# Optimization experiments

Measured on AMD Instinct MI355X. Metric: run time of the kernel, lower is better.

The kernel has to match this reference:

```python
import jax, jax.numpy as jnp
import numpy as np

CURV = 1.0          # manifold curvature c
HEADS = 4
HEAD_DIM = 32       # (dim-1) // heads = 128 // 4
SCALE = HEAD_DIM ** -0.5
EPS = 1e-7

N_NODES = 50000
N_EDGES = 800000
D = 128             # tangent feature dim (dim - 1)


def log_origin(x, c):
    """Lorentz log map at the origin o=(1/sqrt(c),0,...); returns spatial (d) part of tangent."""
    sc = jnp.sqrt(c)
    x0 = x[..., 0]
    xs = x[..., 1:]
    norm = jnp.sqrt(jnp.sum(xs * xs, axis=-1) + EPS)         # (N,)
    dist = jnp.arccosh(jnp.maximum(sc * x0, 1.0 + EPS)) / sc  # (N,)
    return (dist / norm)[..., None] * xs                      # (N, d)


def exp_origin(vs, c):
    """Lorentz exp map at origin of tangent vector (0, vs); returns point (N, d+1)."""
    sc = jnp.sqrt(c)
    r = jnp.sqrt(jnp.sum(vs * vs, axis=-1) + EPS)  # (N,)
    arg = sc * r
    x0 = jnp.cosh(arg) / sc
    xs = (jnp.sinh(arg) / arg)[..., None] * vs
    return jnp.concatenate([x0[..., None], xs], axis=-1)


def setup_inputs() -> dict:
    key = jax.random.key(0)
    k1, k2, k3, k4, k5, k6, k7 = jax.random.split(key, 7)
    # valid hyperboloid points: x0 = sqrt(1/c + ||xs||^2)
    xs = 0.5 * jax.random.normal(k1, (N_NODES, D), dtype=jnp.float32)
    x0 = jnp.sqrt(1.0 / CURV + jnp.sum(xs * xs, axis=-1, keepdims=True))
    x = jnp.concatenate([x0, xs], axis=-1)  # (N, d+1)
    edge_index = jax.random.randint(k2, (2, N_EDGES), 0, N_NODES, dtype=jnp.int64)
    s = D ** -0.5
    Wq = s * jax.random.normal(k3, (D, D), dtype=jnp.float32)
    Wk = s * jax.random.normal(k4, (D, D), dtype=jnp.float32)
    Wv = s * jax.random.normal(k5, (D, D), dtype=jnp.float32)
    Wo = s * jax.random.normal(k6, (D, D), dtype=jnp.float32)
    bo = jnp.zeros((D,), dtype=jnp.float32)
    return {"x": x, "edge_index": edge_index, "Wq": Wq, "Wk": Wk, "Wv": Wv, "Wo": Wo, "bo": bo}


def reference(x, edge_index, Wq, Wk, Wv, Wo, bo):
    N = x.shape[0]
    row, col = edge_index[0], edge_index[1]
    # map to tangent space at origin, drop the (zero) time component
    x_tan = log_origin(x, CURV)                       # (N, d)
    Q = (x_tan @ Wq.T).reshape(N, HEADS, HEAD_DIM)
    K = (x_tan @ Wk.T).reshape(N, HEADS, HEAD_DIM)
    V = (x_tan @ Wv.T).reshape(N, HEADS, HEAD_DIM)
    # per-edge attention logits, grouped softmax over incoming edges of each target node (col)
    scores = jnp.einsum('ehd,ehd->eh', Q[col], K[row]) * SCALE   # (E, H)
    m = jax.ops.segment_max(scores, col, num_segments=N)         # (N, H)
    e = jnp.exp(scores - m[col])
    denom = jax.ops.segment_sum(e, col, num_segments=N)          # (N, H)
    att = e / denom[col]                                         # (E, H)
    # weighted scatter-sum of values
    agg = jax.ops.segment_sum(att[..., None] * V[row], col, num_segments=N)  # (N, H, hd)
    agg = agg.reshape(N, HEADS * HEAD_DIM)
    out = agg @ Wo.T + bo                                        # (N, d)
    # lift back: prepend zero time component, exp map at origin
    return exp_origin(out, CURV)                                 # (N, d+1)
```

## Files before the change

kernel.cpp:

```cpp
#include <hip/hip_runtime.h>
#include <hip/hip_fp8.h>
#include <math.h>

#define EPS 1e-7f
#define SCALE 0.17677669529663687f
#define MAXDEG 64
#define BIN_EPT 16
#define BIN_EDGES 4096
#define BUCK_CAP 5120
#define NBUCK_MAX 256

typedef _Float16 half2v __attribute__((ext_vector_type(2)));
typedef _Float16 f16x4 __attribute__((ext_vector_type(4)));
typedef _Float16 f16x8 __attribute__((ext_vector_type(8)));
typedef float f32x4 __attribute__((ext_vector_type(4)));
typedef float f32x2 __attribute__((ext_vector_type(2)));

__device__ __forceinline__ void gload16(const void* g, void* l) {
  __builtin_amdgcn_global_load_lds(
      (const __attribute__((address_space(1))) unsigned int*)g,
      (__attribute__((address_space(3))) unsigned int*)l, 16, 0, 0);
}

__global__ __launch_bounds__(256) void zero_cnt(int* __restrict__ bcnt, int n) {
  int i = blockIdx.x * 256 + threadIdx.x;
  if (i < n) bcnt[i] = 0;
}

__global__ __launch_bounds__(256) void prep_kernel(
    const float* __restrict__ x,
    const float* __restrict__ Wq, const float* __restrict__ Wk,
    const float* __restrict__ Wv, const float* __restrict__ Wo,
    _Float16* __restrict__ Wc, _Float16* __restrict__ Wof,
    _Float16* __restrict__ xt,
    const int* __restrict__ col, const int* __restrict__ row,
    unsigned* __restrict__ staging, int* __restrict__ bcnt,
    int bin_nb, int nbuck, int E, int N) {
  __shared__ int hist[NBUCK_MAX];
  __shared__ int rbase[NBUCK_MAX];
  int b = blockIdx.x;
  int tid = threadIdx.x;
  if (b < bin_nb) {
    int e0 = b * BIN_EDGES;
    if (tid < nbuck) hist[tid] = 0;
    __syncthreads();
    int bkt[BIN_EPT], rk[BIN_EPT];
    unsigned pk[BIN_EPT];
#pragma unroll
    for (int j = 0; j < BIN_EPT; j++) {
      int e = e0 + j * 256 + tid;
      if (e < E) {
        int c = col[e];
        int r = row[e];
        int bb = c >> 8;
        bkt[j] = bb;
        pk[j] = ((unsigned)(c & 255) << 16) | (unsigned)r;
        rk[j] = atomicAdd(&hist[bb], 1);
      } else {
        bkt[j] = -1;
        rk[j] = 0;
        pk[j] = 0;
      }
    }
    __syncthreads();
    if (tid < nbuck) rbase[tid] = atomicAdd(&bcnt[tid], hist[tid]);
    __syncthreads();
#pragma unroll
    for (int j = 0; j < BIN_EPT; j++) {
      if (bkt[j] >= 0) {
        int slot = rbase[bkt[j]] + rk[j];
        if (slot < BUCK_CAP)
          staging[(size_t)bkt[j] * BUCK_CAP + slot] = pk[j];
      }
    }
    return;
  }
  b -= bin_nb;
  if (b < 256) {
    int o = b * 256 + tid;
    int j = o >> 7;
    int i = o & 127;
    if (j < 384) {
      const float* W = (j < 128) ? Wq : (j < 256) ? Wk : Wv;
      Wc[o] = (_Float16)W[(j & 127) * 128 + i];
    } else {
      Wof[(j - 384) * 128 + i] = (_Float16)Wo[(j - 384) * 128 + i];
    }
    return;
  }
  int node = (b - 256) * 4 + (tid >> 6);
  if (node >= N) return;
  int lane = tid & 63;
  float2 xs = *reinterpret_cast<const float2*>(&x[(size_t)node * 129 + 1 + lane * 2]);
  float ss = fmaf(xs.x, xs.x, xs.y * xs.y);
#pragma unroll
  for (int o = 32; o >= 1; o >>= 1) ss += __shfl_xor(ss, o, 64);
  float norm = sqrtf(ss + EPS);
  float x0 = x[(size_t)node * 129];
  float xm = fmaxf(x0, 1.0f + EPS);
  float dist = __logf(xm + sqrtf(fmaxf(fmaf(xm, xm, -1.0f), 0.0f)));
  float sc = dist / norm;
  half2v h;
  h.x = (_Float16)(sc * xs.x);
  h.y = (_Float16)(sc * xs.y);
  *reinterpret_cast<half2v*>(&xt[(size_t)node * 128 + lane * 2]) = h;
}

template <int NCHUNKS, int MODE>
__global__ __launch_bounds__(256, 3) void gemm_mfma(
    const _Float16* __restrict__ A,
    const _Float16* __restrict__ B,
    void* __restrict__ C0, void* __restrict__ C1,
    const float* __restrict__ bias, int M,
    const unsigned* __restrict__ staging, const int* __restrict__ bcnt,
    unsigned short* __restrict__ rml, int* __restrict__ cnt, int Mblocks) {
  __shared__ _Float16 Bs[128 * 128];
  __shared__ __align__(16) unsigned char Cs[16384];
  const int bid = blockIdx.x;
  const int tid = threadIdx.x;

  if (MODE == 0 && bid >= Mblocks) {
    int bk = bid - Mblocks;
    unsigned short* slab = (unsigned short*)Bs;
    int* lc = (int*)Cs;
    lc[tid] = 0;
    __syncthreads();
    int ec = bcnt[bk];
    if (ec > BUCK_CAP) ec = BUCK_CAP;
    const unsigned* sg = staging + (size_t)bk * BUCK_CAP;
    for (int i = tid; i < ec; i += 256) {
      unsigned p = sg[i];
      int nl = p >> 16;
      int pos = atomicAdd(&lc[nl], 1);
      if (pos < MAXDEG) slab[nl * MAXDEG + pos] = (unsigned short)(p & 0xFFFF);
    }
    __syncthreads();
    uint4* gs = (uint4*)(rml + (size_t)bk * 256 * MAXDEG);
    const uint4* ls = (const uint4*)slab;
#pragma unroll
    for (int i = 0; i < 8; i++) gs[i * 256 + tid] = ls[i * 256 + tid];
    int c = lc[tid];
    cnt[bk * 256 + tid] = (c > MAXDEG) ? MAXDEG : c;
    return;
  }

  const int wave = tid >> 6;
  const int lane = tid & 63;
  const int wm = wave >> 1, wn = wave & 1;
  const int lrow = lane & 15, q = lane >> 4;
  const int m0 = bid * 64;

#pragma unroll
  for (int j = 0; j < 4; j++) {
    int slot0 = (j * 4 + wave) * 64;
    int p = slot0 + lane;
    int m = p >> 4;
    int kcl = (p & 15) ^ (m & 15);
    int msrc = m0 + m;
    if (msrc > M - 1) msrc = M - 1;
    gload16(A + (size_t)msrc * 128 + kcl * 8, (char*)Bs + (size_t)slot0 * 16);
  }
  __syncthreads();

  f16x8 afr[2][4];
  {
    const f16x8* Av = (const f16x8*)Bs;
#pragma unroll
    for (int mt = 0; mt < 2; mt++) {
      int m = wm * 32 + mt * 16 + lrow;
#pragma unroll
      for (int s = 0; s < 4; s++) {
        int kc = s * 4 + q;
        afr[mt][s] = Av[m * 16 + (kc ^ (m & 15))];
      }
    }
  }
  __syncthreads();

  auto stageB = [&](int c) {
#pragma unroll
    for (int j = 0; j < 8; j++) {
      int slot0 = (j * 4 + wave) * 64;
      int p = slot0 + lane;
      int n = p >> 4;
      int kcl = (p & 15) ^ (n & 15);
      gload16(B + ((size_t)(c * 128 + n)) * 128 + kcl * 8, (char*)Bs + (size_t)slot0 * 16);
    }
  };
  stageB(0);

  f32x4 acc[2][4];
  for (int c = 0; c < NCHUNKS; c++) {
    __syncthreads();

#pragma unroll
    for (int mt = 0; mt < 2; mt++)
#pragma unroll
      for (int nt = 0; nt < 4; nt++) acc[mt][nt] = (f32x4)0.f;

    const f16x8* Bv = (const f16x8*)Bs;
#pragma unroll
    for (int s = 0; s < 4; s++) {
      int kc = s * 4 + q;
      f16x8 bf[4];
#pragma unroll
      for (int nt = 0; nt < 4; nt++) {
        int n = wn * 64 + nt * 16 + lrow;
        bf[nt] = Bv[n * 16 + (kc ^ (n & 15))];
      }
#pragma unroll
      for (int mt = 0; mt < 2; mt++)
#pragma unroll
        for (int nt = 0; nt < 4; nt++)
          acc[mt][nt] = __builtin_amdgcn_mfma_f32_16x16x32_f16(afr[mt][s], bf[nt], acc[mt][nt], 0, 0, 0);
    }

    if (MODE == 0) {
      if (c == 0) {
#pragma unroll
        for (int mt = 0; mt < 2; mt++)
#pragma unroll
          for (int reg = 0; reg < 4; reg++) {
            int r = wm * 32 + mt * 16 + q * 4 + reg;
            int sw = ((r >> 2) & 3) << 5;
#pragma unroll
            for (int nt = 0; nt < 4; nt++) {
              int cl = wn * 64 + nt * 16 + lrow;
              *(_Float16*)(Cs + r * 256 + ((cl * 2) ^ sw)) = (_Float16)acc[mt][nt][reg];
            }
          }
      } else {
        unsigned char* cb = Cs + ((c == 2) ? 8192 : 0);
#pragma unroll
        for (int mt = 0; mt < 2; mt++) {
          int rb = wm * 32 + mt * 16 + q * 4;
          int sw = ((rb >> 2) & 3) << 5;
#pragma unroll
          for (int nt = 0; nt < 4; nt++) {
            int cl = wn * 64 + nt * 16 + lrow;
            int co = cl ^ sw;
            int p01 = __builtin_amdgcn_cvt_pk_fp8_f32(acc[mt][nt][0], acc[mt][nt][1], 0, false);
            int p23 = __builtin_amdgcn_cvt_pk_fp8_f32(acc[mt][nt][2], acc[mt][nt][3], 0, false);
            cb[(rb + 0) * 128 + co] = (unsigned char)(p01);
            cb[(rb + 1) * 128 + co] = (unsigned char)(p01 >> 8);
            cb[(rb + 2) * 128 + co] = (unsigned char)(p23);
            cb[(rb + 3) * 128 + co] = (unsigned char)(p23 >> 8);
          }
        }
      }
    }
    __syncthreads();
    if (c + 1 < NCHUNKS) stageB(c + 1);
    if (MODE == 0) {
      if (c == 0) {
#pragma unroll
        for (int it = 0; it < 4; it++) {
          int off = it * 4096 + tid * 16;
          int r = off >> 8;
          int bo = off & 255;
          int sw = ((r >> 2) & 3) << 5;
          uint4 v = *(const uint4*)(Cs + r * 256 + (bo ^ sw));
          int rg = m0 + r;
          if (rg < M) *(uint4*)((char*)C0 + (size_t)rg * 256 + bo) = v;
        }
      } else if (c == 2) {
#pragma unroll
        for (int it = 0; it < 8; it++) {
          int off = it * 2048 + tid * 8;
          int r = off >> 8;
          int u4 = (off & 255) >> 1;
          int sw = ((r >> 2) & 3) << 5;
          unsigned kw = *(const unsigned*)(Cs + r * 128 + (u4 ^ sw));
          unsigned vw = *(const unsigned*)(Cs + 8192 + r * 128 + (u4 ^ sw));
          int rg = m0 + r;
          if (rg < M) {
            uint2 o;
            o.x = kw;
            o.y = vw;
            *(uint2*)((char*)C1 + (size_t)rg * 256 + (off & 255)) = o;
          }
        }
      }
    }
  }

  if (MODE == 1) {
    float* out = (float*)C0;
    float* rsum = (float*)Cs;
#pragma unroll
    for (int mt = 0; mt < 2; mt++)
#pragma unroll
      for (int nt = 0; nt < 4; nt++) {
        int cl = wn * 64 + nt * 16 + lrow;
        float b = bias[cl];
#pragma unroll
        for (int reg = 0; reg < 4; reg++) acc[mt][nt][reg] += b;
      }
#pragma unroll
    for (int mt = 0; mt < 2; mt++) {
#pragma unroll
      for (int reg = 0; reg < 4; reg++) {
        float s4 = 0.f;
#pragma unroll
        for (int nt = 0; nt < 4; nt++) s4 = fmaf(acc[mt][nt][reg], acc[mt][nt][reg], s4);
#pragma unroll
        for (int o = 8; o >= 1; o >>= 1) s4 += __shfl_xor(s4, o, 16);
        if (lrow == 0) rsum[(wm * 32 + mt * 16 + q * 4 + reg) * 2 + wn] = s4;
      }
    }
    __syncthreads();
#pragma unroll
    for (int mt = 0; mt < 2; mt++) {
#pragma unroll
      for (int reg = 0; reg < 4; reg++) {
        int rl = wm * 32 + mt * 16 + q * 4 + reg;
        int rg = m0 + rl;
        if (rg < M) {
          float tot = rsum[rl * 2] + rsum[rl * 2 + 1];
          float r = sqrtf(tot + EPS);
          float er = __expf(r);
          float em = __expf(-r);
          float s = (er - em) * 0.5f / r;
#pragma unroll
          for (int nt = 0; nt < 4; nt++) {
            int cl = wn * 64 + nt * 16 + lrow;
            out[(size_t)rg * 129 + 1 + cl] = s * acc[mt][nt][reg];
          }
          if (wn == 0 && lrow == 0) out[(size_t)rg * 129] = (er + em) * 0.5f;
        }
      }
    }
  }
}

__global__ __launch_bounds__(256) void attn_kernel(
    const _Float16* __restrict__ Qb,
    const unsigned char* __restrict__ KVI,
    const unsigned short* __restrict__ rml, const int* __restrict__ cnt,
    _Float16* __restrict__ agg, int N) {
  int node = blockIdx.x * 4 + (threadIdx.x >> 6);
  if (node >= N) return;
  int lane = threadIdx.x & 63;
  int par = lane >> 5;
  int hd = lane & 31;
  int qoff = hd * 4;
  f16x4 qh = *reinterpret_cast<const f16x4*>(Qb + (size_t)node * 128 + qoff);
  float q0 = (float)qh[0], q1 = (float)qh[1], q2 = (float)qh[2], q3 = (float)qh[3];
  int deg = cnt[node];
  if (deg > MAXDEG) deg = MAXDEG;
  int eid = (int)rml[(size_t)node * MAXDEG + lane];
  float l = 0.f, av0 = 0.f, av1 = 0.f, av2 = 0.f, av3 = 0.f;

  auto dot = [&](uint2 w, float& p, float& v0, float& v1, float& v2, float& v3) {
    f32x2 k01 = __builtin_amdgcn_cvt_pk_f32_fp8((int)w.x, false);
    f32x2 k23 = __builtin_amdgcn_cvt_pk_f32_fp8((int)w.x, true);
    f32x2 va = __builtin_amdgcn_cvt_pk_f32_fp8((int)w.y, false);
    f32x2 vb = __builtin_amdgcn_cvt_pk_f32_fp8((int)w.y, true);
    v0 = va[0]; v1 = va[1]; v2 = vb[0]; v3 = vb[1];
    p = fmaf(q0, k01[0], fmaf(q1, k01[1], fmaf(q2, k23[0], q3 * k23[1])));
  };
  auto ld = [&](int r) {
    return *reinterpret_cast<const uint2*>(KVI + (size_t)r * 256 + hd * 8);
  };
  auto accum4 = [&](uint2 wA, uint2 wB, uint2 wC, uint2 wD) {
    float pA, a4, a5, a6, a7;
    float pB, b4, b5, b6, b7;
    float pC, c4, c5, c6, c7;
    float pD, d4, d5, d6, d7;
    dot(wA, pA, a4, a5, a6, a7);
    dot(wB, pB, b4, b5, b6, b7);
    dot(wC, pC, c4, c5, c6, c7);
    dot(wD, pD, d4, d5, d6, d7);
#pragma unroll
    for (int o = 4; o >= 1; o >>= 1) {
      pA += __shfl_xor(pA, o, 8);
      pB += __shfl_xor(pB, o, 8);
      pC += __shfl_xor(pC, o, 8);
      pD += __shfl_xor(pD, o, 8);
    }
    float eA = __expf(pA * SCALE);
    float eB = __expf(pB * SCALE);
    float eC = __expf(pC * SCALE);
    float eD = __expf(pD * SCALE);
    l += (eA + eB) + (eC + eD);
    av0 = fmaf(eA, a4, av0); av0 = fmaf(eB, b4, av0);
    av1 = fmaf(eA, a5, av1); av1 = fmaf(eB, b5, av1);
    av2 = fmaf(eA, a6, av2); av2 = fmaf(eB, b6, av2);
    av3 = fmaf(eA, a7, av3); av3 = fmaf(eB, b7, av3);
    av0 = fmaf(eC, c4, av0); av0 = fmaf(eD, d4, av0);
    av1 = fmaf(eC, c5, av1); av1 = fmaf(eD, d5, av1);
    av2 = fmaf(eC, c6, av2); av2 = fmaf(eD, d6, av2);
    av3 = fmaf(eC, c7, av3); av3 = fmaf(eD, d7, av3);
  };

  int i = 0;
  for (; i + 16 <= deg; i += 16) {
    int rA = __shfl(eid, i + par, 64);
    int rB = __shfl(eid, i + 2 + par, 64);
    int rC = __shfl(eid, i + 4 + par, 64);
    int rD = __shfl(eid, i + 6 + par, 64);
    int rE = __shfl(eid, i + 8 + par, 64);
    int rF = __shfl(eid, i + 10 + par, 64);
    int rG = __shfl(eid, i + 12 + par, 64);
    int rH = __shfl(eid, i + 14 + par, 64);
    uint2 wA = ld(rA);
    uint2 wB = ld(rB);
    uint2 wC = ld(rC);
    uint2 wD = ld(rD);
    uint2 wE = ld(rE);
    uint2 wF = ld(rF);
    uint2 wG = ld(rG);
    uint2 wH = ld(rH);
    accum4(wA, wB, wC, wD);
    accum4(wE, wF, wG, wH);
  }
  for (; i + 8 <= deg; i += 8) {
    int rA = __shfl(eid, i + par, 64);
    int rB = __shfl(eid, i + 2 + par, 64);
    int rC = __shfl(eid, i + 4 + par, 64);
    int rD = __shfl(eid, i + 6 + par, 64);
    uint2 wA = ld(rA);
    uint2 wB = ld(rB);
    uint2 wC = ld(rC);
    uint2 wD = ld(rD);
    accum4(wA, wB, wC, wD);
  }
  for (; i + 2 <= deg; i += 2) {
    int rA = __shfl(eid, i + par, 64);
    uint2 wA = ld(rA);
    float pA, a4, a5, a6, a7;
    dot(wA, pA, a4, a5, a6, a7);
#pragma unroll
    for (int o = 4; o >= 1; o >>= 1) pA += __shfl_xor(pA, o, 8);
    float eA = __expf(pA * SCALE);
    l += eA;
    av0 = fmaf(eA, a4, av0);
    av1 = fmaf(eA, a5, av1);
    av2 = fmaf(eA, a6, av2);
    av3 = fmaf(eA, a7, av3);
  }
  if (i < deg) {
    int r = __shfl(eid, i, 64);
    uint2 wA = ld(r);
    float pA, a4, a5, a6, a7;
    dot(wA, pA, a4, a5, a6, a7);
#pragma unroll
    for (int o = 4; o >= 1; o >>= 1) pA += __shfl_xor(pA, o, 8);
    float e = __expf(pA * SCALE) * (par ? 0.f : 1.f);
    l += e;
    av0 = fmaf(e, a4, av0);
    av1 = fmaf(e, a5, av1);
    av2 = fmaf(e, a6, av2);
    av3 = fmaf(e, a7, av3);
  }
  l += __shfl_xor(l, 32, 64);
  av0 += __shfl_xor(av0, 32, 64);
  av1 += __shfl_xor(av1, 32, 64);
  av2 += __shfl_xor(av2, 32, 64);
  av3 += __shfl_xor(av3, 32, 64);
  if (par == 0) {
    float inv = (l > 0.f) ? 1.0f / l : 0.f;
    f16x4 o4;
    o4[0] = (_Float16)(av0 * inv);
    o4[1] = (_Float16)(av1 * inv);
    o4[2] = (_Float16)(av2 * inv);
    o4[3] = (_Float16)(av3 * inv);
    *reinterpret_cast<f16x4*>(agg + (size_t)node * 128 + qoff) = o4;
  }
}

extern "C" void kernel_launch(void* const* d_in, const int* in_sizes, int n_in,
                              void* d_out, int out_size, void* d_ws, size_t ws_size,
                              hipStream_t stream) {
  const float* x = (const float*)d_in[0];
  const int* ei = (const int*)d_in[1];
  const float* Wq = (const float*)d_in[2];
  const float* Wk = (const float*)d_in[3];
  const float* Wv = (const float*)d_in[4];
  const float* Wo = (const float*)d_in[5];
  const float* bo = (const float*)d_in[6];
  float* out = (float*)d_out;

  const int N = in_sizes[0] / 129;
  const int E = in_sizes[1] / 2;
  const int* row = ei;
  const int* col = ei + E;

  const int nbuck = (N + 255) >> 8;
  const int bin_nb = (E + BIN_EDGES - 1) / BIN_EDGES;

  char* ws = (char*)d_ws;
  size_t off = 0;
  auto alloc = [&](size_t bytes) -> void* {
    off = (off + 255) & ~(size_t)255;
    void* p = ws + off;
    off += bytes;
    return p;
  };
  _Float16* xtan = (_Float16*)alloc((size_t)N * 128 * 2);
  _Float16* qbuf = (_Float16*)alloc((size_t)N * 128 * 2);
  unsigned char* kvi = (unsigned char*)alloc((size_t)N * 256);
  unsigned short* rml = (unsigned short*)alloc((size_t)nbuck * 256 * MAXDEG * 2);
  int* cnt        = (int*)alloc((size_t)nbuck * 256 * 4);
  unsigned* staging = (unsigned*)alloc((size_t)nbuck * BUCK_CAP * 4);
  int* bcnt       = (int*)alloc((size_t)nbuck * 4);
  _Float16* Wc    = (_Float16*)alloc(384 * 128 * 2);
  _Float16* Wof   = (_Float16*)alloc(128 * 128 * 2);

  const int gemm_nb = (N + 63) / 64;

  zero_cnt<<<(nbuck + 255) / 256, 256, 0, stream>>>(bcnt, nbuck);
  prep_kernel<<<bin_nb + 256 + (N + 3) / 4, 256, 0, stream>>>(
      x, Wq, Wk, Wv, Wo, Wc, Wof, xtan, col, row, staging, bcnt, bin_nb, nbuck,
      E, N);
  gemm_mfma<3, 0><<<gemm_nb + nbuck, 256, 0, stream>>>(
      xtan, Wc, qbuf, kvi, nullptr, N, staging, bcnt, rml, cnt, gemm_nb);
  attn_kernel<<<(N + 3) / 4, 256, 0, stream>>>(qbuf, kvi, rml, cnt, xtan, N);
  gemm_mfma<1, 1><<<gemm_nb, 256, 0, stream>>>(
      xtan, Wof, out, nullptr, bo, N, nullptr, nullptr, nullptr, nullptr, 0);
}
```

Before: 163.7 us.

## Replace global bucket atomics with per-block cells, drop zero kernel, unstage Wo in output GEMM

New measurement: 180.1 us. 10.0% more time.

```diff
diff --git a/kernel.cpp b/kernel.cpp
--- a/kernel.cpp
+++ b/kernel.cpp
@@ -7,7 +7,7 @@
 #define MAXDEG 64
 #define BIN_EPT 16
 #define BIN_EDGES 4096
-#define BUCK_CAP 5120
+#define CELL_CAP 64
 #define NBUCK_MAX 256
 
 typedef _Float16 half2v __attribute__((ext_vector_type(2)));
@@ -20,11 +20,6 @@
   __builtin_amdgcn_global_load_lds(
       (const __attribute__((address_space(1))) unsigned int*)g,
       (__attribute__((address_space(3))) unsigned int*)l, 16, 0, 0);
-}
-
-__global__ __launch_bounds__(256) void zero_cnt(int* __restrict__ bcnt, int n) {
-  int i = blockIdx.x * 256 + threadIdx.x;
-  if (i < n) bcnt[i] = 0;
 }
 
 __global__ __launch_bounds__(256) void prep_kernel(
@@ -34,10 +29,9 @@
     _Float16* __restrict__ Wc, _Float16* __restrict__ Wof,
     _Float16* __restrict__ xt,
     const int* __restrict__ col, const int* __restrict__ row,
-    unsigned* __restrict__ staging, int* __restrict__ bcnt,
+    unsigned* __restrict__ staging, int* __restrict__ ccnt,
     int bin_nb, int nbuck, int E, int N) {
   __shared__ int hist[NBUCK_MAX];
-  __shared__ int rbase[NBUCK_MAX];
   int b = blockIdx.x;
   int tid = threadIdx.x;
   if (b < bin_nb) {
@@ -63,14 +57,11 @@
       }
     }
     __syncthreads();
-    if (tid < nbuck) rbase[tid] = atomicAdd(&bcnt[tid], hist[tid]);
-    __syncthreads();
+    if (tid < nbuck) ccnt[b * NBUCK_MAX + tid] = hist[tid];
 #pragma unroll
     for (int j = 0; j < BIN_EPT; j++) {
-      if (bkt[j] >= 0) {
-        int slot = rbase[bkt[j]] + rk[j];
-        if (slot < BUCK_CAP)
-          staging[(size_t)bkt[j] * BUCK_CAP + slot] = pk[j];
+      if (bkt[j] >= 0 && rk[j] < CELL_CAP) {
+        staging[((size_t)bkt[j] * bin_nb + b) * CELL_CAP + rk[j]] = pk[j];
       }
     }
     return;
@@ -88,22 +79,27 @@
     }
     return;
   }
-  int node = (b - 256) * 4 + (tid >> 6);
+  int node = (b - 256) * 8 + (tid >> 5);
   if (node >= N) return;
-  int lane = tid & 63;
-  float2 xs = *reinterpret_cast<const float2*>(&x[(size_t)node * 129 + 1 + lane * 2]);
-  float ss = fmaf(xs.x, xs.x, xs.y * xs.y);
-#pragma unroll
-  for (int o = 32; o >= 1; o >>= 1) ss += __shfl_xor(ss, o, 64);
+  int sub = tid & 31;
+  const float* xr = x + (size_t)node * 129;
+  float2 xs01 = *reinterpret_cast<const float2*>(xr + 1 + sub * 4);
+  float2 xs23 = *reinterpret_cast<const float2*>(xr + 3 + sub * 4);
+  float ss = fmaf(xs01.x, xs01.x, xs01.y * xs01.y);
+  ss = fmaf(xs23.x, xs23.x, ss);
+  ss = fmaf(xs23.y, xs23.y, ss);
+#pragma unroll
+  for (int o = 16; o >= 1; o >>= 1) ss += __shfl_xor(ss, o, 64);
   float norm = sqrtf(ss + EPS);
-  float x0 = x[(size_t)node * 129];
-  float xm = fmaxf(x0, 1.0f + EPS);
+  float xm = fmaxf(xr[0], 1.0f + EPS);
   float dist = __logf(xm + sqrtf(fmaxf(fmaf(xm, xm, -1.0f), 0.0f)));
   float sc = dist / norm;
-  half2v h;
-  h.x = (_Float16)(sc * xs.x);
-  h.y = (_Float16)(sc * xs.y);
-  *reinterpret_cast<half2v*>(&xt[(size_t)node * 128 + lane * 2]) = h;
+  f16x4 h;
+  h[0] = (_Float16)(sc * xs01.x);
+  h[1] = (_Float16)(sc * xs01.y);
+  h[2] = (_Float16)(sc * xs23.x);
+  h[3] = (_Float16)(sc * xs23.y);
+  *reinterpret_cast<f16x4*>(&xt[(size_t)node * 128 + sub * 4]) = h;
 }
 
 template <int NCHUNKS, int MODE>
@@ -112,9 +108,10 @@
     const _Float16* __restrict__ B,
     void* __restrict__ C0, void* __restrict__ C1,
     const float* __restrict__ bias, int M,
-    const unsigned* __restrict__ staging, const int* __restrict__ bcnt,
-    unsigned short* __restrict__ rml, int* __restrict__ cnt, int Mblocks) {
-  __shared__ _Float16 Bs[128 * 128];
+    const unsigned* __restrict__ staging, const int* __restrict__ ccnt,
+    unsigned short* __restrict__ rml, int* __restrict__ cnt, int Mblocks,
+    int bin_nb) {
+  __shared__ _Float16 Bs[(MODE == 0) ? 128 * 128 : 64 * 128];
   __shared__ __align__(16) unsigned char Cs[16384];
   const int bid = blockIdx.x;
   const int tid = threadIdx.x;
@@ -125,14 +122,18 @@
     int* lc = (int*)Cs;
     lc[tid] = 0;
     __syncthreads();
-    int ec = bcnt[bk];
-    if (ec > BUCK_CAP) ec = BUCK_CAP;
-    const unsigned* sg = staging + (size_t)bk * BUCK_CAP;
-    for (int i = tid; i < ec; i += 256) {
-      unsigned p = sg[i];
-      int nl = p >> 16;
-      int pos = atomicAdd(&lc[nl], 1);
-      if (pos < MAXDEG) slab[nl * MAXDEG + pos] = (unsigned short)(p & 0xFFFF);
+    const unsigned* sg = staging + (size_t)bk * bin_nb * CELL_CAP;
+    int total = bin_nb * CELL_CAP;
+    for (int i = tid; i < total; i += 256) {
+      int blk = i >> 6;
+      int slot = i & (CELL_CAP - 1);
+      int ec = ccnt[blk * NBUCK_MAX + bk];
+      if (slot < ec) {
+        unsigned p = sg[i];
+        int nl = p >> 16;
+        int pos = atomicAdd(&lc[nl], 1);
+        if (pos < MAXDEG) slab[nl * MAXDEG + pos] = (unsigned short)(p & 0xFFFF);
+      }
     }
     __syncthreads();
     uint4* gs = (uint4*)(rml + (size_t)bk * 256 * MAXDEG);
@@ -175,30 +176,14 @@
       }
     }
   }
-  __syncthreads();
-
-  auto stageB = [&](int c) {
-#pragma unroll
-    for (int j = 0; j < 8; j++) {
-      int slot0 = (j * 4 + wave) * 64;
-      int p = slot0 + lane;
-      int n = p >> 4;
-      int kcl = (p & 15) ^ (n & 15);
-      gload16(B + ((size_t)(c * 128 + n)) * 128 + kcl * 8, (char*)Bs + (size_t)slot0 * 16);
-    }
-  };
-  stageB(0);
 
   f32x4 acc[2][4];
-  for (int c = 0; c < NCHUNKS; c++) {
-    __syncthreads();
-
+
+  if (MODE == 1) {
 #pragma unroll
     for (int mt = 0; mt < 2; mt++)
 #pragma unroll
       for (int nt = 0; nt < 4; nt++) acc[mt][nt] = (f32x4)0.f;
-
-    const f16x8* Bv = (const f16x8*)Bs;
 #pragma unroll
     for (int s = 0; s < 4; s++) {
       int kc = s * 4 + q;
@@ -206,7 +191,7 @@
 #pragma unroll
       for (int nt = 0; nt < 4; nt++) {
         int n = wn * 64 + nt * 16 + lrow;
-        bf[nt] = Bv[n * 16 + (kc ^ (n & 15))];
+        bf[nt] = *reinterpret_cast<const f16x8*>(B + (size_t)n * 128 + kc * 8);
       }
 #pragma unroll
       for (int mt = 0; mt < 2; mt++)
@@ -214,77 +199,6 @@
         for (int nt = 0; nt < 4; nt++)
           acc[mt][nt] = __builtin_amdgcn_mfma_f32_16x16x32_f16(afr[mt][s], bf[nt], acc[mt][nt], 0, 0, 0);
     }
-
-    if (MODE == 0) {
-      if (c == 0) {
-#pragma unroll
-        for (int mt = 0; mt < 2; mt++)
-#pragma unroll
-          for (int reg = 0; reg < 4; reg++) {
-            int r = wm * 32 + mt * 16 + q * 4 + reg;
-            int sw = ((r >> 2) & 3) << 5;
-#pragma unroll
-            for (int nt = 0; nt < 4; nt++) {
-              int cl = wn * 64 + nt * 16 + lrow;
-              *(_Float16*)(Cs + r * 256 + ((cl * 2) ^ sw)) = (_Float16)acc[mt][nt][reg];
-            }
-          }
-      } else {
-        unsigned char* cb = Cs + ((c == 2) ? 8192 : 0);
-#pragma unroll
-        for (int mt = 0; mt < 2; mt++) {
-          int rb = wm * 32 + mt * 16 + q * 4;
-          int sw = ((rb >> 2) & 3) << 5;
-#pragma unroll
-          for (int nt = 0; nt < 4; nt++) {
-            int cl = wn * 64 + nt * 16 + lrow;
-            int co = cl ^ sw;
-            int p01 = __builtin_amdgcn_cvt_pk_fp8_f32(acc[mt][nt][0], acc[mt][nt][1], 0, false);
-            int p23 = __builtin_amdgcn_cvt_pk_fp8_f32(acc[mt][nt][2], acc[mt][nt][3], 0, false);
-            cb[(rb + 0) * 128 + co] = (unsigned char)(p01);
-            cb[(rb + 1) * 128 + co] = (unsigned char)(p01 >> 8);
-            cb[(rb + 2) * 128 + co] = (unsigned char)(p23);
-            cb[(rb + 3) * 128 + co] = (unsigned char)(p23 >> 8);
-          }
-        }
-      }
-    }
-    __syncthreads();
-    if (c + 1 < NCHUNKS) stageB(c + 1);
-    if (MODE == 0) {
-      if (c == 0) {
-#pragma unroll
-        for (int it = 0; it < 4; it++) {
-          int off = it * 4096 + tid * 16;
-          int r = off >> 8;
-          int bo = off & 255;
-          int sw = ((r >> 2) & 3) << 5;
-          uint4 v = *(const uint4*)(Cs + r * 256 + (bo ^ sw));
-          int rg = m0 + r;
-          if (rg < M) *(uint4*)((char*)C0 + (size_t)rg * 256 + bo) = v;
-        }
-      } else if (c == 2) {
-#pragma unroll
-        for (int it = 0; it < 8; it++) {
-          int off = it * 2048 + tid * 8;
-          int r = off >> 8;
-          int u4 = (off & 255) >> 1;
-          int sw = ((r >> 2) & 3) << 5;
-          unsigned kw = *(const unsigned*)(Cs + r * 128 + (u4 ^ sw));
-          unsigned vw = *(const unsigned*)(Cs + 8192 + r * 128 + (u4 ^ sw));
-          int rg = m0 + r;
-          if (rg < M) {
-            uint2 o;
-            o.x = kw;
-            o.y = vw;
-            *(uint2*)((char*)C1 + (size_t)rg * 256 + (off & 255)) = o;
-          }
-        }
-      }
-    }
-  }
-
-  if (MODE == 1) {
     float* out = (float*)C0;
     float* rsum = (float*)Cs;
 #pragma unroll
@@ -292,9 +206,9 @@
 #pragma unroll
       for (int nt = 0; nt < 4; nt++) {
         int cl = wn * 64 + nt * 16 + lrow;
-        float b = bias[cl];
-#pragma unroll
-        for (int reg = 0; reg < 4; reg++) acc[mt][nt][reg] += b;
+        float bb = bias[cl];
+#pragma unroll
+        for (int reg = 0; reg < 4; reg++) acc[mt][nt][reg] += bb;
       }
 #pragma unroll
     for (int mt = 0; mt < 2; mt++) {
@@ -327,6 +241,111 @@
             out[(size_t)rg * 129 + 1 + cl] = s * acc[mt][nt][reg];
           }
           if (wn == 0 && lrow == 0) out[(size_t)rg * 129] = (er + em) * 0.5f;
+        }
+      }
+    }
+    return;
+  }
+
+  __syncthreads();
+
+  auto stageB = [&](int c) {
+#pragma unroll
+    for (int j = 0; j < 8; j++) {
+      int slot0 = (j * 4 + wave) * 64;
+      int p = slot0 + lane;
+      int n = p >> 4;
+      int kcl = (p & 15) ^ (n & 15);
+      gload16(B + ((size_t)(c * 128 + n)) * 128 + kcl * 8, (char*)Bs + (size_t)slot0 * 16);
+    }
+  };
+  stageB(0);
+
+  for (int c = 0; c < NCHUNKS; c++) {
+    __syncthreads();
+
+#pragma unroll
+    for (int mt = 0; mt < 2; mt++)
+#pragma unroll
+      for (int nt = 0; nt < 4; nt++) acc[mt][nt] = (f32x4)0.f;
+
+    const f16x8* Bv = (const f16x8*)Bs;
+#pragma unroll
+    for (int s = 0; s < 4; s++) {
+      int kc = s * 4 + q;
+      f16x8 bf[4];
+#pragma unroll
+      for (int nt = 0; nt < 4; nt++) {
+        int n = wn * 64 + nt * 16 + lrow;
+        bf[nt] = Bv[n * 16 + (kc ^ (n & 15))];
+      }
+#pragma unroll
+      for (int mt = 0; mt < 2; mt++)
+#pragma unroll
+        for (int nt = 0; nt < 4; nt++)
+          acc[mt][nt] = __builtin_amdgcn_mfma_f32_16x16x32_f16(afr[mt][s], bf[nt], acc[mt][nt], 0, 0, 0);
+    }
+
+    if (c == 0) {
+#pragma unroll
+      for (int mt = 0; mt < 2; mt++)
+#pragma unroll
+        for (int reg = 0; reg < 4; reg++) {
+          int r = wm * 32 + mt * 16 + q * 4 + reg;
+          int sw = ((r >> 2) & 3) << 5;
+#pragma unroll
+          for (int nt = 0; nt < 4; nt++) {
+            int cl = wn * 64 + nt * 16 + lrow;
+            *(_Float16*)(Cs + r * 256 + ((cl * 2) ^ sw)) = (_Float16)acc[mt][nt][reg];
+          }
+        }
+    } else {
+      unsigned char* cb = Cs + ((c == 2) ? 8192 : 0);
+#pragma unroll
+      for (int mt = 0; mt < 2; mt++) {
+        int rb = wm * 32 + mt * 16 + q * 4;
+        int sw = ((rb >> 2) & 3) << 5;
+#pragma unroll
+        for (int nt = 0; nt < 4; nt++) {
+          int cl = wn * 64 + nt * 16 + lrow;
+          int co = cl ^ sw;
+          int p01 = __builtin_amdgcn_cvt_pk_fp8_f32(acc[mt][nt][0], acc[mt][nt][1], 0, false);
+          int p23 = __builtin_amdgcn_cvt_pk_fp8_f32(acc[mt][nt][2], acc[mt][nt][3], 0, false);
+          cb[(rb + 0) * 128 + co] = (unsigned char)(p01);
+          cb[(rb + 1) * 128 + co] = (unsigned char)(p01 >> 8);
+          cb[(rb + 2) * 128 + co] = (unsigned char)(p23);
+          cb[(rb + 3) * 128 + co] = (unsigned char)(p23 >> 8);
+        }
+      }
+    }
+    __syncthreads();
+    if (c + 1 < NCHUNKS) stageB(c + 1);
+    if (c == 0) {
+#pragma unroll
+      for (int it = 0; it < 4; it++) {
+        int off = it * 4096 + tid * 16;
+        int r = off >> 8;
+        int bo = off & 255;
+        int sw = ((r >> 2) & 3) << 5;
+        uint4 v = *(const uint4*)(Cs + r * 256 + (bo ^ sw));
+        int rg = m0 + r;
+        if (rg < M) *(uint4*)((char*)C0 + (size_t)rg * 256 + bo) = v;
+      }
+    } else if (c == 2) {
+#pragma unroll
+      for (int it = 0; it < 8; it++) {
+        int off = it * 2048 + tid * 8;
+        int r = off >> 8;
+        int u4 = (off & 255) >> 1;
+        int sw = ((r >> 2) & 3) << 5;
+        unsigned kw = *(const unsigned*)(Cs + r * 128 + (u4 ^ sw));
+        unsigned vw = *(const unsigned*)(Cs + 8192 + r * 128 + (u4 ^ sw));
+        int rg = m0 + r;
+        if (rg < M) {
+          uint2 o;
+          o.x = kw;
+          o.y = vw;
+          *(uint2*)((char*)C1 + (size_t)rg * 256 + (off & 255)) = o;
         }
       }
     }
@@ -502,20 +521,19 @@
   unsigned char* kvi = (unsigned char*)alloc((size_t)N * 256);
   unsigned short* rml = (unsigned short*)alloc((size_t)nbuck * 256 * MAXDEG * 2);
   int* cnt        = (int*)alloc((size_t)nbuck * 256 * 4);
-  unsigned* staging = (unsigned*)alloc((size_t)nbuck * BUCK_CAP * 4);
-  int* bcnt       = (int*)alloc((size_t)nbuck * 4);
+  unsigned* staging = (unsigned*)alloc((size_t)nbuck * bin_nb * CELL_CAP * 4);
+  int* ccnt       = (int*)alloc((size_t)bin_nb * NBUCK_MAX * 4);
   _Float16* Wc    = (_Float16*)alloc(384 * 128 * 2);
   _Float16* Wof   = (_Float16*)alloc(128 * 128 * 2);
 
   const int gemm_nb = (N + 63) / 64;
 
-  zero_cnt<<<(nbuck + 255) / 256, 256, 0, stream>>>(bcnt, nbuck);
-  prep_kernel<<<bin_nb + 256 + (N + 3) / 4, 256, 0, stream>>>(
-      x, Wq, Wk, Wv, Wo, Wc, Wof, xtan, col, row, staging, bcnt, bin_nb, nbuck,
+  prep_kernel<<<bin_nb + 256 + (N + 7) / 8, 256, 0, stream>>>(
+      x, Wq, Wk, Wv, Wo, Wc, Wof, xtan, col, row, staging, ccnt, bin_nb, nbuck,
       E, N);
   gemm_mfma<3, 0><<<gemm_nb + nbuck, 256, 0, stream>>>(
-      xtan, Wc, qbuf, kvi, nullptr, N, staging, bcnt, rml, cnt, gemm_nb);
+      xtan, Wc, qbuf, kvi, nullptr, N, staging, ccnt, rml, cnt, gemm_nb, bin_nb);
   attn_kernel<<<(N + 3) / 4, 256, 0, stream>>>(qbuf, kvi, rml, cnt, xtan, N);
   gemm_mfma<1, 1><<<gemm_nb, 256, 0, stream>>>(
-      xtan, Wof, out, nullptr, bo, N, nullptr, nullptr, nullptr, nullptr, 0);
+      xtan, Wof, out, nullptr, bo, N, nullptr, nullptr, nullptr, nullptr, 0, 0);
 }
```
